# Performance work log

Measured on AMD Instinct MI355X. Metric: run time of the kernel, lower is better.

Reference implementation:

```python
import jax, jax.numpy as jnp
import numpy as np

NUM_CLASSES = 512  # P distinct identities in the batch (labels are in [0, P))
TAU = 0.5
EPS = 1e-12


def _l2norm(x):
    # F.normalize(x, dim=1) with eps clamp
    n = jnp.sqrt(jnp.sum(x * x, axis=1, keepdims=True))
    return x / jnp.maximum(n, EPS)


def setup_inputs() -> dict:
    key = jax.random.key(0)
    k1, k2, k3 = jax.random.split(key, 3)
    N, D, P = 8192, 2048, NUM_CLASSES
    feat_vp = jax.random.normal(k1, (N, D), dtype=jnp.float32)
    feat_ap = jax.random.normal(k2, (N, D), dtype=jnp.float32)
    feat_rp = jax.random.normal(k3, (N, D), dtype=jnp.float32)
    # P identities, K = N/P instances each; every class present
    label = (jnp.arange(N) % P).astype(jnp.int32)
    return {"feat_vp": feat_vp, "feat_ap": feat_ap, "feat_rp": feat_rp, "label": label}


def reference(feat_vp, feat_ap, feat_rp, label):
    P = NUM_CLASSES
    fv = _l2norm(feat_vp)
    fa = _l2norm(feat_ap)
    fr = _l2norm(feat_rp)

    # segment-mean over labels (replaces the O(N^2 D) python loop)
    counts = jax.ops.segment_sum(jnp.ones_like(label, dtype=fv.dtype), label,
                                 num_segments=P)  # [P]
    inv_cnt = 1.0 / counts[:, None]

    def centers(f):
        s = jax.ops.segment_sum(f, label, num_segments=P)  # [P, D]
        return _l2norm(s * inv_cnt)

    cv, ca, cr = centers(fv), centers(fa), centers(fr)

    # per-sample centers = unique centers gathered back by label
    loss_intra = (jnp.sum((fv - cv[label]) ** 2, axis=1).mean()
                  + jnp.sum((fa - ca[label]) ** 2, axis=1).mean()
                  + jnp.sum((fr - cr[label]) ** 2, axis=1).mean())

    def pair_loss(c1, c2):
        logits = (c1 @ c2.T) / TAU  # [P, P]
        logp = jax.nn.log_softmax(logits, axis=1)
        return -jnp.mean(jnp.diagonal(logp))

    loss_inter = pair_loss(cv, ca) + pair_loss(cv, cr) + pair_loss(ca, cr)
    return loss_intra + loss_inter
```

## Files before the change

### kernel.cpp

```cpp
#include <hip/hip_runtime.h>
#include <hip/hip_bf16.h>

#define P_CLS 512
#define D_DIM 2048
#define CAP   32
#define TAU_INV 2.0f

typedef short short8 __attribute__((ext_vector_type(8)));
typedef float f32x4 __attribute__((ext_vector_type(4)));

__device__ __forceinline__ unsigned short f2bf_bits(float x) {
  __hip_bfloat16 b = __float2bfloat16(x);
  unsigned short u;
  __builtin_memcpy(&u, &b, sizeof(u));
  return u;
}

__device__ __forceinline__ void async16(const void* g, void* l) {
  __builtin_amdgcn_global_load_lds(
      (const __attribute__((address_space(1))) void*)g,
      (__attribute__((address_space(3))) void*)l, 16, 0, 0);
}

__device__ __forceinline__ float xred_sum(float v) {
#pragma unroll
  for (int o = 1; o < 64; o <<= 1) v += __shfl_xor(v, o, 64);
  return v;
}
__device__ __forceinline__ float xred_max(float v) {
#pragma unroll
  for (int o = 1; o < 64; o <<= 1) v = fmaxf(v, __shfl_xor(v, o, 64));
  return v;
}

__global__ void k_init(int* cnt, float* accs) {
  int t = blockIdx.x * blockDim.x + threadIdx.x;
  if (t < P_CLS) cnt[t] = 0;
  if (t < 8) accs[t] = 0.f;
}

__global__ void k_index(const int* __restrict__ label, int* __restrict__ cnt,
                        int* __restrict__ idx, int n) {
  int i = blockIdx.x * blockDim.x + threadIdx.x;
  if (i < n) {
    int p = label[i];
    int slot = atomicAdd(&cnt[p], 1);
    if (slot < CAP) idx[p * CAP + slot] = i;
  }
}

__global__ __launch_bounds__(256)
void k_centers(const float* __restrict__ f0, const float* __restrict__ f1,
               const float* __restrict__ f2, const int* __restrict__ cnt,
               const int* __restrict__ idx, __hip_bfloat16* __restrict__ cb,
               float* __restrict__ accs) {
  __shared__ __align__(16) float rows[8 * D_DIM];
  __shared__ float scr[16];
  int p = blockIdx.x, m = blockIdx.y;
  const float* F = (m == 0) ? f0 : (m == 1) ? f1 : f2;
  int t = threadIdx.x, lane = t & 63, wv = t >> 6;
  int c = cnt[p];
  if (c > CAP) c = CAP;
  const int* idxp = idx + p * CAP;

  f32x4 acc0 = {0, 0, 0, 0}, acc1 = {0, 0, 0, 0};
  for (int base = 0; base < c; base += 8) {
#pragma unroll
    for (int s = 0; s < 2; ++s) {
      int rr = 2 * wv + s, gr = base + rr;
      if (gr < c) {
        const char* rowp = (const char*)(F + (long)idxp[gr] * D_DIM);
        char* ldsp = (char*)(rows + rr * D_DIM);
#pragma unroll
        for (int j = 0; j < 8; ++j)
          async16(rowp + j * 1024 + lane * 16, ldsp + j * 1024 + lane * 16);
      }
    }
    __syncthreads();
#pragma unroll
    for (int s = 0; s < 2; ++s) {
      int rr = 2 * wv + s;
      const f32x4* rp = (const f32x4*)(rows + rr * D_DIM);
      float ssq = 0.f;
#pragma unroll
      for (int j = 0; j < 8; ++j) {
        f32x4 q = rp[lane + 64 * j];
        q = q * q;
        ssq += q.x + q.y + q.z + q.w;
      }
      ssq = xred_sum(ssq);
      if (lane == 0)
        scr[rr] = (base + rr < c) ? (1.0f / fmaxf(sqrtf(ssq), 1e-12f)) : 0.f;
    }
    __syncthreads();
#pragma unroll
    for (int rr = 0; rr < 8; ++rr) {
      float w = scr[rr];
      f32x4 x0 = *(const f32x4*)(rows + rr * D_DIM + t * 4);
      f32x4 x1 = *(const f32x4*)(rows + rr * D_DIM + 1024 + t * 4);
      acc0 += x0 * w;
      acc1 += x1 * w;
    }
    __syncthreads();
  }
  f32x4 q0 = acc0 * acc0, q1 = acc1 * acc1;
  float s2 = q0.x + q0.y + q0.z + q0.w + q1.x + q1.y + q1.z + q1.w;
  s2 = xred_sum(s2);
  if (lane == 0) scr[8 + wv] = s2;
  __syncthreads();
  s2 = scr[8] + scr[9] + scr[10] + scr[11];
  float sn = sqrtf(s2);
  float inv = 1.0f / fmaxf(sn, 1e-12f);
  __hip_bfloat16* dst = cb + ((long)m * P_CLS + p) * D_DIM;
  f32x4 o0 = acc0 * inv, o1 = acc1 * inv;
  ushort4 h0, h1;
  h0.x = f2bf_bits(o0.x); h0.y = f2bf_bits(o0.y);
  h0.z = f2bf_bits(o0.z); h0.w = f2bf_bits(o0.w);
  h1.x = f2bf_bits(o1.x); h1.y = f2bf_bits(o1.y);
  h1.z = f2bf_bits(o1.z); h1.w = f2bf_bits(o1.w);
  ((ushort4*)dst)[t] = h0;
  ((ushort4*)dst)[t + 256] = h1;
  if (t == 0 && c > 0) atomicAdd(&accs[0], sn);
}

__global__ __launch_bounds__(256)
void k_gemm(const __hip_bfloat16* __restrict__ cbh, float* __restrict__ logits) {
  __shared__ __align__(16) unsigned short As[2][64 * 40], Bs[2][64 * 40];
  int pair = blockIdx.y, kz = blockIdx.z, nkz = gridDim.z;
  int ksl = D_DIM / nkz;
  int ma = (pair == 2) ? 1 : 0;
  int mb = (pair == 0) ? 1 : 2;
  const unsigned short* A =
      (const unsigned short*)cbh + (long)ma * P_CLS * D_DIM + kz * ksl;
  const unsigned short* B =
      (const unsigned short*)cbh + (long)mb * P_CLS * D_DIM + kz * ksl;
  float* C = logits + ((long)kz * 3 + pair) * P_CLS * P_CLS;
  int tm = (blockIdx.x >> 3) * 64, tn = (blockIdx.x & 7) * 64;
  int t = threadIdx.x, lane = t & 63, wv = t >> 6;
  int srow = t >> 2, skc = (t & 3) * 8;
  int quad = lane >> 4, mr = lane & 15;
  const unsigned short* pa = A + (long)(tm + srow) * D_DIM + skc;
  const unsigned short* pb = B + (long)(tn + srow) * D_DIM + skc;
  f32x4 acc[4] = {{0,0,0,0},{0,0,0,0},{0,0,0,0},{0,0,0,0}};
  uint4 av = *(const uint4*)pa, bv = *(const uint4*)pb;
  *(uint4*)(&As[0][srow * 40 + skc]) = av;
  *(uint4*)(&Bs[0][srow * 40 + skc]) = bv;
  av = *(const uint4*)(pa + 32); bv = *(const uint4*)(pb + 32);
  const int NIT = ksl / 32;
  for (int it = 0; it < NIT; ++it) {
    __syncthreads();
    int cur = it & 1;
    if (it + 1 < NIT) {
      *(uint4*)(&As[cur ^ 1][srow * 40 + skc]) = av;
      *(uint4*)(&Bs[cur ^ 1][srow * 40 + skc]) = bv;
    }
    if (it + 2 < NIT) {
      av = *(const uint4*)(pa + (it + 2) * 32);
      bv = *(const uint4*)(pb + (it + 2) * 32);
    }
    short8 af = *(const short8*)(&As[cur][(wv * 16 + mr) * 40 + quad * 8]);
#pragma unroll
    for (int nb = 0; nb < 4; ++nb) {
      short8 bfr = *(const short8*)(&Bs[cur][(nb * 16 + mr) * 40 + quad * 8]);
      acc[nb] = __builtin_amdgcn_mfma_f32_16x16x32_bf16(af, bfr, acc[nb], 0, 0, 0);
    }
  }
  int crow = tm + wv * 16 + quad * 4;
#pragma unroll
  for (int nb = 0; nb < 4; ++nb)
#pragma unroll
    for (int r = 0; r < 4; ++r)
      C[(long)(crow + r) * P_CLS + tn + nb * 16 + mr] = acc[nb][r] * TAU_INV;
}

__global__ __launch_bounds__(256)
void k_lse(const float* __restrict__ logits, float* __restrict__ accs, int nkz) {
  __shared__ float sred[8];
  int row = blockIdx.x;
  int p = row & (P_CLS - 1);
  int t = threadIdx.x, lane = t & 63, wv = t >> 6;
  float v0 = 0.f, v1 = 0.f, diag = 0.f;
  for (int z = 0; z < nkz; ++z) {
    const float* L = logits + ((long)z * 3 * P_CLS + row) * P_CLS;
    v0 += L[t];
    v1 += L[t + 256];
  }
  float mx = xred_max(fmaxf(v0, v1));
  if (lane == 0) sred[wv] = mx;
  __syncthreads();
  mx = fmaxf(fmaxf(sred[0], sred[1]), fmaxf(sred[2], sred[3]));
  float e = expf(v0 - mx) + expf(v1 - mx);
  e = xred_sum(e);
  if (lane == 0) sred[4 + wv] = e;
  __syncthreads();
  if (t == 0) {
    float tot = sred[4] + sred[5] + sred[6] + sred[7];
    for (int z = 0; z < nkz; ++z)
      diag += logits[((long)z * 3 * P_CLS + row) * P_CLS + p];
    atomicAdd(&accs[1], mx + logf(tot) - diag);
  }
}

__global__ void k_final(const float* __restrict__ accs, float* __restrict__ out,
                        float invN) {
  out[0] = 6.0f - 2.0f * invN * accs[0] + accs[1] * (1.0f / (float)P_CLS);
}

extern "C" void kernel_launch(void* const* d_in, const int* in_sizes, int n_in,
                              void* d_out, int out_size, void* d_ws, size_t ws_size,
                              hipStream_t stream) {
  const float* fvp = (const float*)d_in[0];
  const float* fap = (const float*)d_in[1];
  const float* frp = (const float*)d_in[2];
  const int* label = (const int*)d_in[3];
  int N = in_sizes[3];

  char* ws = (char*)d_ws;
  int* cnt = (int*)ws;
  int* idx = (int*)(ws + 2048);
  float* accs = (float*)(ws + 2048 + 65536);
  __hip_bfloat16* cb = (__hip_bfloat16*)(ws + 131072);
  float* logits = (float*)(ws + 131072 + 3ul * P_CLS * D_DIM * 2);

  size_t base = 131072 + 3ul * P_CLS * D_DIM * 2;
  size_t per_z = 3ul * P_CLS * P_CLS * 4;
  int KZ = (ws_size >= base + 4 * per_z) ? 4 : 2;

  hipLaunchKernelGGL(k_init, dim3(1), dim3(512), 0, stream, cnt, accs);
  hipLaunchKernelGGL(k_index, dim3((N + 255) / 256), dim3(256), 0, stream,
                     label, cnt, idx, N);
  hipLaunchKernelGGL(k_centers, dim3(P_CLS, 3), dim3(256), 0, stream,
                     fvp, fap, frp, cnt, idx, cb, accs);
  hipLaunchKernelGGL(k_gemm, dim3(64, 3, KZ), dim3(256), 0, stream, cb, logits);
  hipLaunchKernelGGL(k_lse, dim3(3 * P_CLS), dim3(256), 0, stream, logits, accs, KZ);
  hipLaunchKernelGGL(k_final, dim3(1), dim3(1), 0, stream, accs, (float*)d_out,
                     1.0f / (float)N);
}
```

Before: 239.0 us.

## Stream center rows through registers with per-wave double buffering, reduce via LDS

The centers kernel no longer stages 8 rows into LDS with async loads and three barriers per batch. Each wave now owns every fourth row, loads it straight into registers with a two-row software prefetch, normalizes it and accumulates it locally. The four per-wave partial sums are combined through LDS once at the end. This removes repeated block-wide syncs and LDS round trips, at the cost of more registers and a final cross-wave reduction.

```diff
diff --git a/kernel.cpp b/kernel.cpp
--- a/kernel.cpp
+++ b/kernel.cpp
@@ -14,12 +14,6 @@
   unsigned short u;
   __builtin_memcpy(&u, &b, sizeof(u));
   return u;
-}
-
-__device__ __forceinline__ void async16(const void* g, void* l) {
-  __builtin_amdgcn_global_load_lds(
-      (const __attribute__((address_space(1))) void*)g,
-      (__attribute__((address_space(3))) void*)l, 16, 0, 0);
 }
 
 __device__ __forceinline__ float xred_sum(float v) {
@@ -54,8 +48,8 @@
                const float* __restrict__ f2, const int* __restrict__ cnt,
                const int* __restrict__ idx, __hip_bfloat16* __restrict__ cb,
                float* __restrict__ accs) {
-  __shared__ __align__(16) float rows[8 * D_DIM];
-  __shared__ float scr[16];
+  __shared__ __align__(16) f32x4 red[4][D_DIM / 4];
+  __shared__ float scr[4];
   int p = blockIdx.x, m = blockIdx.y;
   const float* F = (m == 0) ? f0 : (m == 1) ? f1 : f2;
   int t = threadIdx.x, lane = t & 63, wv = t >> 6;
@@ -63,56 +57,56 @@
   if (c > CAP) c = CAP;
   const int* idxp = idx + p * CAP;
 
-  f32x4 acc0 = {0, 0, 0, 0}, acc1 = {0, 0, 0, 0};
-  for (int base = 0; base < c; base += 8) {
-#pragma unroll
-    for (int s = 0; s < 2; ++s) {
-      int rr = 2 * wv + s, gr = base + rr;
-      if (gr < c) {
-        const char* rowp = (const char*)(F + (long)idxp[gr] * D_DIM);
-        char* ldsp = (char*)(rows + rr * D_DIM);
-#pragma unroll
-        for (int j = 0; j < 8; ++j)
-          async16(rowp + j * 1024 + lane * 16, ldsp + j * 1024 + lane * 16);
-      }
-    }
-    __syncthreads();
-#pragma unroll
-    for (int s = 0; s < 2; ++s) {
-      int rr = 2 * wv + s;
-      const f32x4* rp = (const f32x4*)(rows + rr * D_DIM);
-      float ssq = 0.f;
-#pragma unroll
-      for (int j = 0; j < 8; ++j) {
-        f32x4 q = rp[lane + 64 * j];
-        q = q * q;
-        ssq += q.x + q.y + q.z + q.w;
-      }
-      ssq = xred_sum(ssq);
-      if (lane == 0)
-        scr[rr] = (base + rr < c) ? (1.0f / fmaxf(sqrtf(ssq), 1e-12f)) : 0.f;
-    }
-    __syncthreads();
-#pragma unroll
-    for (int rr = 0; rr < 8; ++rr) {
-      float w = scr[rr];
-      f32x4 x0 = *(const f32x4*)(rows + rr * D_DIM + t * 4);
-      f32x4 x1 = *(const f32x4*)(rows + rr * D_DIM + 1024 + t * 4);
-      acc0 += x0 * w;
-      acc1 += x1 * w;
-    }
-    __syncthreads();
-  }
-  f32x4 q0 = acc0 * acc0, q1 = acc1 * acc1;
+  int nr = (c > wv) ? ((c - wv + 3) >> 2) : 0;
+
+  f32x4 acc[8] = {{0,0,0,0},{0,0,0,0},{0,0,0,0},{0,0,0,0},
+                  {0,0,0,0},{0,0,0,0},{0,0,0,0},{0,0,0,0}};
+  f32x4 a[8], b[8];
+
+  auto loadrow = [&](f32x4* buf, int r) {
+    const f32x4* rp = (const f32x4*)(F + (long)idxp[r] * D_DIM);
+#pragma unroll
+    for (int j = 0; j < 8; ++j) buf[j] = rp[lane + 64 * j];
+  };
+  auto consume = [&](const f32x4* buf) {
+    float ssq = 0.f;
+#pragma unroll
+    for (int j = 0; j < 8; ++j) {
+      f32x4 q = buf[j] * buf[j];
+      ssq += q.x + q.y + q.z + q.w;
+    }
+    ssq = xred_sum(ssq);
+    float w = 1.0f / fmaxf(sqrtf(ssq), 1e-12f);
+#pragma unroll
+    for (int j = 0; j < 8; ++j) acc[j] += buf[j] * w;
+  };
+
+  if (nr > 0) loadrow(a, wv);
+  if (nr > 1) loadrow(b, wv + 4);
+  for (int k = 0; k < nr; k += 2) {
+    consume(a);
+    if (k + 2 < nr) loadrow(a, wv + 4 * (k + 2));
+    if (k + 1 < nr) {
+      consume(b);
+      if (k + 3 < nr) loadrow(b, wv + 4 * (k + 3));
+    }
+  }
+
+#pragma unroll
+  for (int j = 0; j < 8; ++j) red[wv][lane + 64 * j] = acc[j];
+  __syncthreads();
+  f32x4 s0 = red[0][t] + red[1][t] + red[2][t] + red[3][t];
+  f32x4 s1 = red[0][t + 256] + red[1][t + 256] + red[2][t + 256] + red[3][t + 256];
+  f32x4 q0 = s0 * s0, q1 = s1 * s1;
   float s2 = q0.x + q0.y + q0.z + q0.w + q1.x + q1.y + q1.z + q1.w;
   s2 = xred_sum(s2);
-  if (lane == 0) scr[8 + wv] = s2;
-  __syncthreads();
-  s2 = scr[8] + scr[9] + scr[10] + scr[11];
+  if (lane == 0) scr[wv] = s2;
+  __syncthreads();
+  s2 = scr[0] + scr[1] + scr[2] + scr[3];
   float sn = sqrtf(s2);
   float inv = 1.0f / fmaxf(sn, 1e-12f);
   __hip_bfloat16* dst = cb + ((long)m * P_CLS + p) * D_DIM;
-  f32x4 o0 = acc0 * inv, o1 = acc1 * inv;
+  f32x4 o0 = s0 * inv, o1 = s1 * inv;
   ushort4 h0, h1;
   h0.x = f2bf_bits(o0.x); h0.y = f2bf_bits(o0.y);
   h0.z = f2bf_bits(o0.z); h0.w = f2bf_bits(o0.w);
```

Result: no change. 238.7 us (-0.1%).
